# Performance work log

Measured on AMD Instinct MI355X. Metric: run time of the kernel, lower is better.

Reference implementation:

```python
import jax, jax.numpy as jnp
import numpy as np

E, B, F, L = 4, 8192, 2048, 100  # envs, batch/env, feature dim, num classes
LAM = 1.0  # hparams['RERM_lam']


def setup_inputs() -> dict:
    key = jax.random.key(0)
    k1, k2, k3 = jax.random.split(key, 3)
    feats = jax.random.normal(k1, (E, B, F), jnp.float32)
    y = jax.random.randint(k2, (E, B), 0, L)
    W = jax.random.normal(k3, (F, L), jnp.float32) * 0.02
    b = jnp.zeros((L,), jnp.float32)
    return {"feats": feats, "y": y, "W": W, "b": b}


def _rerm_loss(feats, y, W, b):
    # --- per-(label, env) masked means (mean_table / visit_table) ---
    onehot = jax.nn.one_hot(y, L, dtype=feats.dtype)          # [E,B,L]
    counts = onehot.sum(axis=1)                               # [E,L]
    sums = jnp.einsum('ebl,ebf->elf', onehot, feats)          # [E,L,F]
    means = sums / jnp.maximum(counts, 1.0)[..., None]        # [E,L,F]
    visit = (counts > 0).astype(feats.dtype)                  # [E,L]

    # --- torch.var(mean_table[i, fetch_envs, :], dim=1): variance over
    # feature dim per env (unbiased, /(F-1)), then mean over visited envs ---
    mu = means.mean(axis=-1, keepdims=True)                   # [E,L,1]
    var = jnp.sum((means - mu) ** 2, axis=-1) / (F - 1)       # [E,L]

    nvis = visit.sum(axis=0)                                  # [L]
    sel = (nvis > 1.5).astype(feats.dtype)                    # labels with >1 env
    per_label = (var * visit).sum(axis=0) / jnp.maximum(nvis, 1.0)  # [L]
    nzlabel = jnp.maximum(sel.sum(), 1.0)
    mean_loss = LAM * jnp.sum(per_label * sel) / nzlabel

    # --- cross-entropy over all envs concatenated ---
    logits = feats.reshape(E * B, F) @ W + b                  # [E*B,L]
    logp = jax.nn.log_softmax(logits, axis=-1)
    ce = -jnp.take_along_axis(logp, y.reshape(-1, 1), axis=1).mean()

    return mean_loss + ce


def reference(feats, y, W, b):
    return _rerm_loss(feats, y, W, b)
```

## Files before the change

### kernel.cpp

```cpp
#include <hip/hip_runtime.h>
#include <hip/hip_bf16.h>
#include <math.h>

#define E 4
#define B 8192
#define F 2048
#define L 100
#define NROWS (E * B)
#define LAMBDA 1.0f

typedef __attribute__((ext_vector_type(8))) short bf16x8;
typedef __attribute__((ext_vector_type(4))) float f32x4;

static __device__ inline unsigned short f2bf(float x) {
    unsigned u = __float_as_uint(x);
    unsigned r = (u + 0x7FFFu + ((u >> 16) & 1u)) >> 16;
    return (unsigned short)r;
}

#define SG 4
#define NSG 25
#define SBS 8
#define SRW (B / SBS)
#define NSUM (E * SBS * NSG)

#define GBM 32
#define GKC 64
#define APAD 72
#define NGEMM (NROWS / GBM)
#define NBASE 115
#define NBLK (NBASE * 16)

__global__ void __launch_bounds__(256) k_prep(const float* __restrict__ W,
                                              unsigned short* __restrict__ Wt,
                                              float* __restrict__ ce_accum,
                                              int* __restrict__ counts) {
    __shared__ float st[64][101];
    int t = threadIdx.x;
    int b = blockIdx.x;
    if (b == 0) {
        for (int i = t; i < E * L; i += 256) counts[i] = 0;
        if (t == 0) ce_accum[0] = 0.f;
    }
    int k0 = b * 64;
    for (int i = t; i < 64 * 100; i += 256) {
        st[i / 100][i % 100] = W[(size_t)k0 * L + i];
    }
    __syncthreads();
    for (int i = t; i < 112 * 32; i += 256) {
        int n = i >> 5, kp = i & 31;
        unsigned lo = 0, hi = 0;
        if (n < L) {
            lo = f2bf(st[kp * 2][n]);
            hi = f2bf(st[kp * 2 + 1][n]);
        }
        *(unsigned*)&Wt[(size_t)n * F + k0 + kp * 2] = lo | (hi << 16);
    }
}

static __device__ inline unsigned pack_bf(float lo, float hi) {
    unsigned ul = __float_as_uint(lo) + 0x8000u;
    unsigned uh = __float_as_uint(hi) + 0x8000u;
    return __builtin_amdgcn_perm(uh, ul, 0x07060302u);
}

__global__ void __launch_bounds__(512, 8) k_main(const float* __restrict__ feats,
                                                 const int* __restrict__ y,
                                                 const unsigned short* __restrict__ Wt,
                                                 const float* __restrict__ bias,
                                                 float* __restrict__ partial,
                                                 int* __restrict__ counts,
                                                 float* __restrict__ ce_accum) {
    __shared__ __align__(16) char sm[22400];
    int t = threadIdx.x;
    int u = blockIdx.x;
    int br = u & 15, base = u >> 4;

    if (br < 9) {
        int gid = base * 9 + br;
        if (gid >= NGEMM) return;
        unsigned short* As = (unsigned short*)sm;
        unsigned short* Ws = As + GBM * APAD;
        float* pmaxs = (float*)(sm + 20736);
        float* psums = pmaxs + 128;
        float* ptgts = psums + 128;
        float* ceg   = ptgts + 128;
        int wave = t >> 6, lane = t & 63;
        int quad = lane >> 4, l16 = lane & 15;
        int g = wave >> 2, h = wave & 3;
        size_t row0 = (size_t)gid * GBM;

        int arow = t >> 4, acol = (t & 15) * 4;
        const float* aptr = feats + (row0 + arow) * (size_t)F + acol;
        int w1row = t >> 3, w1c = (t & 7) * 8;
        int w2row = (512 + t) >> 3, w2c = ((512 + t) & 7) * 8;
        const unsigned short* wp1 = Wt + (size_t)w1row * F + w1c;
        const unsigned short* wp2 = (t < 384) ? Wt + (size_t)w2row * F + w2c : Wt;

        f32x4 acc0 = (f32x4){0.f, 0.f, 0.f, 0.f};
        f32x4 acc1 = acc0;

        float4 pa = *(const float4*)aptr;
        uint4 pw1 = *(const uint4*)wp1;
        uint4 pw2 = *(const uint4*)wp2;

        for (int k0 = 0; k0 < F; k0 += GKC) {
            __syncthreads();
            unsigned u0 = pack_bf(pa.x, pa.y), u1 = pack_bf(pa.z, pa.w);
            *(uint2*)&As[arow * APAD + acol] = make_uint2(u0, u1);
            *(uint4*)&Ws[w1row * APAD + w1c] = pw1;
            if (t < 384) *(uint4*)&Ws[w2row * APAD + w2c] = pw2;
            __syncthreads();
            if (k0 + GKC < F) {
                pa  = *(const float4*)(aptr + k0 + GKC);
                pw1 = *(const uint4*)(wp1 + k0 + GKC);
                pw2 = *(const uint4*)(wp2 + k0 + GKC);
            }
#pragma unroll
            for (int ks = 0; ks < 2; ++ks) {
                bf16x8 bfr = *(const bf16x8*)&As[(g * 16 + l16) * APAD + ks * 32 + quad * 8];
                bf16x8 af0 = *(const bf16x8*)&Ws[((2 * h) * 16 + l16) * APAD + ks * 32 + quad * 8];
                acc0 = __builtin_amdgcn_mfma_f32_16x16x32_bf16(af0, bfr, acc0, 0, 0, 0);
                if (h < 3) {
                    bf16x8 af1 = *(const bf16x8*)&Ws[((2 * h + 1) * 16 + l16) * APAD + ks * 32 + quad * 8];
                    acc1 = __builtin_amdgcn_mfma_f32_16x16x32_bf16(af1, bfr, acc1, 0, 0, 0);
                }
            }
        }

        int rl = g * 16 + l16;
        int lab = y[row0 + rl];
        float vv[2][4];
        float vm = -1e30f;
#pragma unroll
        for (int j = 0; j < 2; ++j) {
#pragma unroll
            for (int r = 0; r < 4; ++r) {
                int ct = 2 * h + j;
                int c = ct * 16 + quad * 4 + r;
                float v = (j == 0) ? acc0[r] : acc1[r];
                float bb = (c < L) ? bias[c] : 0.f;
                v += bb;
                vv[j][r] = v;
                bool valid = (c < L) && (j == 0 || h < 3);
                if (valid) vm = fmaxf(vm, v);
            }
        }
        vm = fmaxf(vm, __shfl_xor(vm, 16));
        vm = fmaxf(vm, __shfl_xor(vm, 32));
        if (lane < 16) pmaxs[h * 32 + rl] = vm;
        __syncthreads();
        float M = fmaxf(fmaxf(pmaxs[rl], pmaxs[32 + rl]),
                        fmaxf(pmaxs[64 + rl], pmaxs[96 + rl]));
        float se = 0.f, tv = 0.f;
#pragma unroll
        for (int j = 0; j < 2; ++j) {
#pragma unroll
            for (int r = 0; r < 4; ++r) {
                int ct = 2 * h + j;
                int c = ct * 16 + quad * 4 + r;
                bool valid = (c < L) && (j == 0 || h < 3);
                if (valid) se += __expf(vv[j][r] - M);
                if (valid && c == lab) tv += vv[j][r];
            }
        }
        se += __shfl_xor(se, 16);
        se += __shfl_xor(se, 32);
        tv += __shfl_xor(tv, 16);
        tv += __shfl_xor(tv, 32);
        if (lane < 16) { psums[h * 32 + rl] = se; ptgts[h * 32 + rl] = tv; }
        __syncthreads();
        if (h == 0 && lane < 16) {
            float SE = psums[rl] + psums[32 + rl] + psums[64 + rl] + psums[96 + rl];
            float TV = ptgts[rl] + ptgts[32 + rl] + ptgts[64 + rl] + ptgts[96 + rl];
            float ce = M + __logf(SE) - TV;
            ce += __shfl_xor(ce, 1);
            ce += __shfl_xor(ce, 2);
            ce += __shfl_xor(ce, 4);
            ce += __shfl_xor(ce, 8);
            if (lane == 0) ceg[g] = ce;
        }
        __syncthreads();
        if (t == 0) atomicAdd(ce_accum, ceg[0] + ceg[1]);
    } else {
        int sid = base * 7 + (br - 9);
        if (sid >= NSUM) return;
        int* ys = (int*)sm;
        unsigned short* list = (unsigned short*)(sm + 4096);
        int* cnt4 = (int*)(sm + 4096 + 2048);
        int* ntot = (int*)(sm + 4096 + 2048 + 16);
        int lg = sid % NSG;
        int bs = (sid / NSG) % SBS;
        int e  = sid / (NSG * SBS);
        int lab0 = lg * SG;

        if (t < SG) cnt4[t] = 0;
        if (t == 8) ntot[0] = 0;
        const int* yb = y + e * B + bs * SRW;
        ys[t] = yb[t];
        ys[t + 512] = yb[t + 512];
        __syncthreads();

        for (int r = t; r < SRW; r += 512) {
            int lb = ys[r] - lab0;
            if ((unsigned)lb < SG) {
                atomicAdd(&cnt4[lb], 1);
                int p = atomicAdd(ntot, 1);
                list[p] = (unsigned short)(r | (lb << 10));
            }
        }
        __syncthreads();
        int n = ntot[0];
        int npad = (n + 3) & ~3;
        if (t < npad - n) list[n + t] = 0;
        __syncthreads();

        const float* fb = feats + ((size_t)e * B + (size_t)bs * SRW) * F + t * 4;
        float4 a0 = make_float4(0.f, 0.f, 0.f, 0.f);
        float4 a1 = a0, a2 = a0, a3 = a0;

        float4 x[4];
        int tg[4];
        if (n > 0) {
#pragma unroll
            for (int j = 0; j < 4; ++j) {
                int ev = list[j];
                tg[j] = ev >> 10;
                x[j] = *(const float4*)(fb + (size_t)(ev & 1023) * F);
            }
            for (int i = 0; i < npad; i += 4) {
                float4 nx[4];
                int ntg[4];
                if (i + 4 < npad) {
#pragma unroll
                    for (int j = 0; j < 4; ++j) {
                        int ev = list[i + 4 + j];
                        ntg[j] = ev >> 10;
                        nx[j] = *(const float4*)(fb + (size_t)(ev & 1023) * F);
                    }
                }
#pragma unroll
                for (int j = 0; j < 4; ++j) {
                    if (i + j < n) {
                        float4 v = x[j];
                        int g2 = tg[j];
                        if (g2 == 0)      { a0.x += v.x; a0.y += v.y; a0.z += v.z; a0.w += v.w; }
                        else if (g2 == 1) { a1.x += v.x; a1.y += v.y; a1.z += v.z; a1.w += v.w; }
                        else if (g2 == 2) { a2.x += v.x; a2.y += v.y; a2.z += v.z; a2.w += v.w; }
                        else              { a3.x += v.x; a3.y += v.y; a3.z += v.z; a3.w += v.w; }
                    }
                }
#pragma unroll
                for (int j = 0; j < 4; ++j) { x[j] = nx[j]; tg[j] = ntg[j]; }
            }
        }

        float* pb = partial + (((size_t)e * SBS + bs) * L + lab0) * F + t * 4;
        *(float4*)(pb + 0 * F) = a0;
        *(float4*)(pb + 1 * F) = a1;
        *(float4*)(pb + 2 * F) = a2;
        *(float4*)(pb + 3 * F) = a3;
        if (t < SG) atomicAdd(&counts[e * L + lab0 + t], cnt4[t]);
    }
}

__global__ void __launch_bounds__(512) k_var(const float* __restrict__ partial,
                                             const int* __restrict__ counts,
                                             float* __restrict__ var_out) {
    int el = blockIdx.x;
    int e = el / L, l = el % L;
    int t = threadIdx.x;
    float inv = 1.f / fmaxf((float)counts[el], 1.f);
    float4 s = make_float4(0.f, 0.f, 0.f, 0.f);
#pragma unroll
    for (int bs = 0; bs < SBS; ++bs) {
        float4 v = *(const float4*)&partial[(((size_t)e * SBS + bs) * L + l) * F + t * 4];
        s.x += v.x; s.y += v.y; s.z += v.z; s.w += v.w;
    }
    float mx = s.x * inv, my = s.y * inv, mz = s.z * inv, mw = s.w * inv;
    float sm = mx + my + mz + mw;
    float sm2 = mx * mx + my * my + mz * mz + mw * mw;
#pragma unroll
    for (int sft = 1; sft <= 32; sft <<= 1) {
        sm += __shfl_xor(sm, sft);
        sm2 += __shfl_xor(sm2, sft);
    }
    __shared__ float r1[8], r2[8];
    int wv = t >> 6, ln = t & 63;
    if (ln == 0) { r1[wv] = sm; r2[wv] = sm2; }
    __syncthreads();
    if (t == 0) {
        float S = 0.f, S2 = 0.f;
#pragma unroll
        for (int w = 0; w < 8; ++w) { S += r1[w]; S2 += r2[w]; }
        var_out[el] = (S2 - S * S / (float)F) / (float)(F - 1);
    }
}

__global__ void k_final(const int* __restrict__ counts,
                        const float* __restrict__ var_in,
                        const float* __restrict__ ce_accum,
                        float* __restrict__ out) {
    __shared__ float s_sum[128], s_cnt[128];
    int t = threadIdx.x;
    float selsum = 0.f, selcnt = 0.f;
    for (int l = t; l < L; l += 128) {
        float nvis = 0.f, vsum = 0.f;
        for (int e = 0; e < E; ++e) {
            if (counts[e * L + l] > 0) { nvis += 1.f; vsum += var_in[e * L + l]; }
        }
        float per_label = vsum / fmaxf(nvis, 1.f);
        if (nvis > 1.5f) { selsum += per_label; selcnt += 1.f; }
    }
    s_sum[t] = selsum; s_cnt[t] = selcnt;
    __syncthreads();
    for (int s = 64; s > 0; s >>= 1) {
        if (t < s) { s_sum[t] += s_sum[t + s]; s_cnt[t] += s_cnt[t + s]; }
        __syncthreads();
    }
    if (t == 0) {
        float mean_loss = LAMBDA * s_sum[0] / fmaxf(s_cnt[0], 1.f);
        float ce = ce_accum[0] / (float)NROWS;
        out[0] = mean_loss + ce;
    }
}

extern "C" void kernel_launch(void* const* d_in, const int* in_sizes, int n_in,
                              void* d_out, int out_size, void* d_ws, size_t ws_size,
                              hipStream_t stream) {
    const float* feats = (const float*)d_in[0];
    const int*   y     = (const int*)d_in[1];
    const float* Wm    = (const float*)d_in[2];
    const float* bias  = (const float*)d_in[3];
    float* out = (float*)d_out;

    char* ws = (char*)d_ws;
    float*          ce_accum = (float*)ws;
    int*            counts   = (int*)(ws + 256);
    float*          var_buf  = (float*)(ws + 2048);
    float*          partial  = (float*)(ws + 4096);
    unsigned short* Wt       = (unsigned short*)(ws + 4096 + (size_t)E * SBS * L * F * 4);

    k_prep<<<F / 64, 256, 0, stream>>>(Wm, Wt, ce_accum, counts);
    k_main<<<NBLK, 512, 0, stream>>>(feats, y, Wt, bias, partial, counts, ce_accum);
    k_var<<<E * L, 512, 0, stream>>>(partial, counts, var_buf);
    k_final<<<1, 128, 0, stream>>>(counts, var_buf, ce_accum, out);
}
```

Baseline: 413.2 us.

## Fuse per-label variance into sum blocks and drop partial-sum buffer

The label-sum blocks now each own two labels of one environment and loop over all 8 row chunks themselves. Because a block holds the complete per-label sums, it can compute the mean and variance directly and write var/counts, so the k_var kernel and the large partial-sum buffer go away. The interleaved GEMM/sum block mapping is replaced by placing all sum blocks first, followed by the GEMM blocks. The trade-off is far fewer sum blocks (200 instead of 800), each running a long serial chunk loop with extra barriers, and each block now scans all label data per chunk for only two labels. That could leave a long tail of slow sum blocks while the GEMM work runs.

```diff
diff --git a/kernel.cpp b/kernel.cpp
--- a/kernel.cpp
+++ b/kernel.cpp
@@ -18,30 +18,25 @@
     return (unsigned short)r;
 }
 
-#define SG 4
-#define NSG 25
-#define SBS 8
-#define SRW (B / SBS)
-#define NSUM (E * SBS * NSG)
+#define SG 2
+#define NSG 50
+#define NCHUNK 8
+#define CRW 1024
+#define NSUMB (E * NSG)
 
 #define GBM 32
 #define GKC 64
 #define APAD 72
 #define NGEMM (NROWS / GBM)
-#define NBASE 115
-#define NBLK (NBASE * 16)
+#define NBLK (NSUMB + NGEMM)
 
 __global__ void __launch_bounds__(256) k_prep(const float* __restrict__ W,
                                               unsigned short* __restrict__ Wt,
-                                              float* __restrict__ ce_accum,
-                                              int* __restrict__ counts) {
+                                              float* __restrict__ ce_accum) {
     __shared__ float st[64][101];
     int t = threadIdx.x;
     int b = blockIdx.x;
-    if (b == 0) {
-        for (int i = t; i < E * L; i += 256) counts[i] = 0;
-        if (t == 0) ce_accum[0] = 0.f;
-    }
+    if (b == 0 && t == 0) ce_accum[0] = 0.f;
     int k0 = b * 64;
     for (int i = t; i < 64 * 100; i += 256) {
         st[i / 100][i % 100] = W[(size_t)k0 * L + i];
@@ -68,17 +63,14 @@
                                                  const int* __restrict__ y,
                                                  const unsigned short* __restrict__ Wt,
                                                  const float* __restrict__ bias,
-                                                 float* __restrict__ partial,
                                                  int* __restrict__ counts,
+                                                 float* __restrict__ var_out,
                                                  float* __restrict__ ce_accum) {
     __shared__ __align__(16) char sm[22400];
     int t = threadIdx.x;
-    int u = blockIdx.x;
-    int br = u & 15, base = u >> 4;
-
-    if (br < 9) {
-        int gid = base * 9 + br;
-        if (gid >= NGEMM) return;
+
+    if (blockIdx.x >= NSUMB) {
+        int gid = blockIdx.x - NSUMB;
         unsigned short* As = (unsigned short*)sm;
         unsigned short* Ws = As + GBM * APAD;
         float* pmaxs = (float*)(sm + 20736);
@@ -183,45 +175,51 @@
         __syncthreads();
         if (t == 0) atomicAdd(ce_accum, ceg[0] + ceg[1]);
     } else {
-        int sid = base * 7 + (br - 9);
-        if (sid >= NSUM) return;
+        int sid = blockIdx.x;
+        int lg = sid % NSG;
+        int e  = sid / NSG;
+        int lab0 = lg * SG;
+
         int* ys = (int*)sm;
         unsigned short* list = (unsigned short*)(sm + 4096);
-        int* cnt4 = (int*)(sm + 4096 + 2048);
-        int* ntot = (int*)(sm + 4096 + 2048 + 16);
-        int lg = sid % NSG;
-        int bs = (sid / NSG) % SBS;
-        int e  = sid / (NSG * SBS);
-        int lab0 = lg * SG;
-
-        if (t < SG) cnt4[t] = 0;
-        if (t == 8) ntot[0] = 0;
-        const int* yb = y + e * B + bs * SRW;
-        ys[t] = yb[t];
-        ys[t + 512] = yb[t + 512];
-        __syncthreads();
-
-        for (int r = t; r < SRW; r += 512) {
-            int lb = ys[r] - lab0;
-            if ((unsigned)lb < SG) {
-                atomicAdd(&cnt4[lb], 1);
-                int p = atomicAdd(ntot, 1);
-                list[p] = (unsigned short)(r | (lb << 10));
-            }
-        }
-        __syncthreads();
-        int n = ntot[0];
-        int npad = (n + 3) & ~3;
-        if (t < npad - n) list[n + t] = 0;
-        __syncthreads();
-
-        const float* fb = feats + ((size_t)e * B + (size_t)bs * SRW) * F + t * 4;
+        int* cnt2 = (int*)(sm + 6144);
+        int* ntot = (int*)(sm + 6144 + 8);
+        int* cntT = (int*)(sm + 6144 + 16);
+        float* rr  = (float*)(sm + 6144 + 32);
+
+        if (t < SG) cntT[t] = 0;
+
         float4 a0 = make_float4(0.f, 0.f, 0.f, 0.f);
-        float4 a1 = a0, a2 = a0, a3 = a0;
-
-        float4 x[4];
-        int tg[4];
-        if (n > 0) {
+        float4 a1 = a0;
+
+        for (int c = 0; c < NCHUNK; ++c) {
+            __syncthreads();
+            if (t < SG) cnt2[t] = 0;
+            if (t == 8) ntot[0] = 0;
+            const int* yb = y + e * B + c * CRW;
+            ys[t] = yb[t];
+            ys[t + 512] = yb[t + 512];
+            __syncthreads();
+
+            for (int r = t; r < CRW; r += 512) {
+                int lb = ys[r] - lab0;
+                if ((unsigned)lb < SG) {
+                    atomicAdd(&cnt2[lb], 1);
+                    int p = atomicAdd(ntot, 1);
+                    list[p] = (unsigned short)(r | (lb << 10));
+                }
+            }
+            __syncthreads();
+            int n = ntot[0];
+            if (t < SG) cntT[t] += cnt2[t];
+            int npad = (n + 3) & ~3;
+            if (t < npad - n) list[n + t] = 0;
+            __syncthreads();
+            if (n == 0) continue;
+
+            const float* fb = feats + ((size_t)e * B + (size_t)c * CRW) * F + t * 4;
+            float4 x[4];
+            int tg[4];
 #pragma unroll
             for (int j = 0; j < 4; ++j) {
                 int ev = list[j];
@@ -243,57 +241,47 @@
                 for (int j = 0; j < 4; ++j) {
                     if (i + j < n) {
                         float4 v = x[j];
-                        int g2 = tg[j];
-                        if (g2 == 0)      { a0.x += v.x; a0.y += v.y; a0.z += v.z; a0.w += v.w; }
-                        else if (g2 == 1) { a1.x += v.x; a1.y += v.y; a1.z += v.z; a1.w += v.w; }
-                        else if (g2 == 2) { a2.x += v.x; a2.y += v.y; a2.z += v.z; a2.w += v.w; }
-                        else              { a3.x += v.x; a3.y += v.y; a3.z += v.z; a3.w += v.w; }
+                        if (tg[j] == 0) { a0.x += v.x; a0.y += v.y; a0.z += v.z; a0.w += v.w; }
+                        else            { a1.x += v.x; a1.y += v.y; a1.z += v.z; a1.w += v.w; }
                     }
                 }
 #pragma unroll
                 for (int j = 0; j < 4; ++j) { x[j] = nx[j]; tg[j] = ntg[j]; }
             }
         }
-
-        float* pb = partial + (((size_t)e * SBS + bs) * L + lab0) * F + t * 4;
-        *(float4*)(pb + 0 * F) = a0;
-        *(float4*)(pb + 1 * F) = a1;
-        *(float4*)(pb + 2 * F) = a2;
-        *(float4*)(pb + 3 * F) = a3;
-        if (t < SG) atomicAdd(&counts[e * L + lab0 + t], cnt4[t]);
-    }
-}
-
-__global__ void __launch_bounds__(512) k_var(const float* __restrict__ partial,
-                                             const int* __restrict__ counts,
-                                             float* __restrict__ var_out) {
-    int el = blockIdx.x;
-    int e = el / L, l = el % L;
-    int t = threadIdx.x;
-    float inv = 1.f / fmaxf((float)counts[el], 1.f);
-    float4 s = make_float4(0.f, 0.f, 0.f, 0.f);
-#pragma unroll
-    for (int bs = 0; bs < SBS; ++bs) {
-        float4 v = *(const float4*)&partial[(((size_t)e * SBS + bs) * L + l) * F + t * 4];
-        s.x += v.x; s.y += v.y; s.z += v.z; s.w += v.w;
-    }
-    float mx = s.x * inv, my = s.y * inv, mz = s.z * inv, mw = s.w * inv;
-    float sm = mx + my + mz + mw;
-    float sm2 = mx * mx + my * my + mz * mz + mw * mw;
-#pragma unroll
-    for (int sft = 1; sft <= 32; sft <<= 1) {
-        sm += __shfl_xor(sm, sft);
-        sm2 += __shfl_xor(sm2, sft);
-    }
-    __shared__ float r1[8], r2[8];
-    int wv = t >> 6, ln = t & 63;
-    if (ln == 0) { r1[wv] = sm; r2[wv] = sm2; }
-    __syncthreads();
-    if (t == 0) {
-        float S = 0.f, S2 = 0.f;
-#pragma unroll
-        for (int w = 0; w < 8; ++w) { S += r1[w]; S2 += r2[w]; }
-        var_out[el] = (S2 - S * S / (float)F) / (float)(F - 1);
+        __syncthreads();
+
+        float inv0 = 1.f / fmaxf((float)cntT[0], 1.f);
+        float inv1 = 1.f / fmaxf((float)cntT[1], 1.f);
+        float m0x = a0.x * inv0, m0y = a0.y * inv0, m0z = a0.z * inv0, m0w = a0.w * inv0;
+        float m1x = a1.x * inv1, m1y = a1.y * inv1, m1z = a1.z * inv1, m1w = a1.w * inv1;
+        float s0 = m0x + m0y + m0z + m0w;
+        float q0 = m0x * m0x + m0y * m0y + m0z * m0z + m0w * m0w;
+        float s1 = m1x + m1y + m1z + m1w;
+        float q1 = m1x * m1x + m1y * m1y + m1z * m1z + m1w * m1w;
+#pragma unroll
+        for (int sft = 1; sft <= 32; sft <<= 1) {
+            s0 += __shfl_xor(s0, sft);
+            q0 += __shfl_xor(q0, sft);
+            s1 += __shfl_xor(s1, sft);
+            q1 += __shfl_xor(q1, sft);
+        }
+        int wv = t >> 6, ln = t & 63;
+        if (ln == 0) {
+            rr[wv] = s0; rr[8 + wv] = q0; rr[16 + wv] = s1; rr[24 + wv] = q1;
+        }
+        __syncthreads();
+        if (t == 0) {
+            float S0 = 0.f, Q0 = 0.f, S1 = 0.f, Q1 = 0.f;
+#pragma unroll
+            for (int w = 0; w < 8; ++w) {
+                S0 += rr[w]; Q0 += rr[8 + w]; S1 += rr[16 + w]; Q1 += rr[24 + w];
+            }
+            var_out[e * L + lab0]     = (Q0 - S0 * S0 / (float)F) / (float)(F - 1);
+            var_out[e * L + lab0 + 1] = (Q1 - S1 * S1 / (float)F) / (float)(F - 1);
+            counts[e * L + lab0]     = cntT[0];
+            counts[e * L + lab0 + 1] = cntT[1];
+        }
     }
 }
 
@@ -338,11 +326,9 @@
     float*          ce_accum = (float*)ws;
     int*            counts   = (int*)(ws + 256);
     float*          var_buf  = (float*)(ws + 2048);
-    float*          partial  = (float*)(ws + 4096);
-    unsigned short* Wt       = (unsigned short*)(ws + 4096 + (size_t)E * SBS * L * F * 4);
-
-    k_prep<<<F / 64, 256, 0, stream>>>(Wm, Wt, ce_accum, counts);
-    k_main<<<NBLK, 512, 0, stream>>>(feats, y, Wt, bias, partial, counts, ce_accum);
-    k_var<<<E * L, 512, 0, stream>>>(partial, counts, var_buf);
+    unsigned short* Wt       = (unsigned short*)(ws + 4096);
+
+    k_prep<<<F / 64, 256, 0, stream>>>(Wm, Wt, ce_accum);
+    k_main<<<NBLK, 512, 0, stream>>>(feats, y, Wt, bias, counts, var_buf, ce_accum);
     k_final<<<1, 128, 0, stream>>>(counts, var_buf, ce_accum, out);
 }
```

After: 400.4 us. 3.1% less time.
